# Performance work log

Hardware: AMD Instinct MI355X
Metric: run time of the kernel (lower is better)

Reference implementation:

```python
import jax, jax.numpy as jnp
import numpy as np

STRIDE = 4
N_LAYERS = 4
N_HEADS = 8
D_MODEL = 1024
D_FF = 4096
WINDOW = 400 // STRIDE      # lookback window (in folded frames)
LOOKFWD = 80 // STRIDE      # lookforward (in folded frames)
ROPE_BASE = 10000.0


def _layernorm(x, scale, bias, eps=1e-5):
    mu = jnp.mean(x, axis=-1, keepdims=True)
    var = jnp.mean(jnp.square(x - mu), axis=-1, keepdims=True)
    return (x - mu) * jax.lax.rsqrt(var + eps) * scale + bias


def _rope(x):
    # x: [B, H, S, Dh]
    B, H, S, Dh = x.shape
    half = Dh // 2
    inv_freq = 1.0 / (ROPE_BASE ** (jnp.arange(half, dtype=jnp.float32) / half))
    ang = jnp.arange(S, dtype=jnp.float32)[:, None] * inv_freq[None, :]  # [S, half]
    cos = jnp.cos(ang).astype(x.dtype)
    sin = jnp.sin(ang).astype(x.dtype)
    x1, x2 = x[..., :half], x[..., half:]
    return jnp.concatenate([x1 * cos - x2 * sin, x1 * sin + x2 * cos], axis=-1)


def setup_inputs() -> dict:
    key = jax.random.key(0)
    ks = jax.random.split(key, 32)
    B, T, C = 4, 4096, 512
    L, D, F = N_LAYERS, D_MODEL, D_FF
    s = 0.02
    inp = {
        'x': jax.random.normal(ks[0], (B, T, C), dtype=jnp.float32),
        'x_lengths': jax.random.randint(ks[1], (B,), 0, T + 1, dtype=jnp.int64 if jax.config.jax_enable_x64 else jnp.int32),
        'Wp': jax.random.normal(ks[2], (C * STRIDE, D), dtype=jnp.float32) * s,
        'bp': jnp.zeros((D,), jnp.float32),
        'ln1_s': jnp.ones((L, D), jnp.float32), 'ln1_b': jnp.zeros((L, D), jnp.float32),
        'Wq': jax.random.normal(ks[3], (L, D, D), jnp.float32) * s, 'bq': jnp.zeros((L, D), jnp.float32),
        'Wk': jax.random.normal(ks[4], (L, D, D), jnp.float32) * s, 'bk': jnp.zeros((L, D), jnp.float32),
        'Wv': jax.random.normal(ks[5], (L, D, D), jnp.float32) * s, 'bv': jnp.zeros((L, D), jnp.float32),
        'Wo': jax.random.normal(ks[6], (L, D, D), jnp.float32) * s, 'bo': jnp.zeros((L, D), jnp.float32),
        'ln2_s': jnp.ones((L, D), jnp.float32), 'ln2_b': jnp.zeros((L, D), jnp.float32),
        'W1': jax.random.normal(ks[7], (L, D, F), jnp.float32) * s, 'b1': jnp.zeros((L, F), jnp.float32),
        'W2': jax.random.normal(ks[8], (L, F, D), jnp.float32) * s, 'b2': jnp.zeros((L, D), jnp.float32),
        'lnf_s': jnp.ones((D,), jnp.float32), 'lnf_b': jnp.zeros((D,), jnp.float32),
    }
    return inp


def reference(x, x_lengths, Wp, bp, ln1_s, ln1_b, Wq, bq, Wk, bk, Wv, bv, Wo, bo,
              ln2_s, ln2_b, W1, b1, W2, b2, lnf_s, lnf_b):
    B, T, C = x.shape
    S = T // STRIDE
    H, Dh = N_HEADS, D_MODEL // N_HEADS
    # stride-fold + input projection
    xf = x[:, :S * STRIDE].reshape(B, S, C * STRIDE)
    h = xf @ Wp + bp                                  # [B, S, D]
    lens = x_lengths // STRIDE
    pad = (jnp.arange(S)[None, :] < lens[:, None])    # [B, S] valid-key mask
    h = h * pad[:, :, None].astype(h.dtype)
    # sliding-window causal-with-lookforward mask + key padding
    i = jnp.arange(S)[:, None]
    j = jnp.arange(S)[None, :]
    win = (j - i <= LOOKFWD) & (i - j < WINDOW)       # [S, S]
    allowed = win[None, None] & pad[:, None, None, :] # [B, 1, S, S]
    bias = jnp.where(allowed, 0.0, -1e9).astype(h.dtype)
    scale = 1.0 / jnp.sqrt(jnp.asarray(Dh, h.dtype))
    for l in range(N_LAYERS):
        # --- pre-LN RoPE windowed attention ---
        y = _layernorm(h, ln1_s[l], ln1_b[l])
        q = (y @ Wq[l] + bq[l]).reshape(B, S, H, Dh).transpose(0, 2, 1, 3)
        k = (y @ Wk[l] + bk[l]).reshape(B, S, H, Dh).transpose(0, 2, 1, 3)
        v = (y @ Wv[l] + bv[l]).reshape(B, S, H, Dh).transpose(0, 2, 1, 3)
        q, k = _rope(q), _rope(k)
        scores = jnp.einsum('bhqe,bhke->bhqk', q, k) * scale + bias
        attn = jax.nn.softmax(scores, axis=-1)
        ctx = jnp.einsum('bhqk,bhke->bhqe', attn, v)
        ctx = ctx.transpose(0, 2, 1, 3).reshape(B, S, D_MODEL)
        h = h + ctx @ Wo[l] + bo[l]
        # --- pre-LN FFN (kernel_size=1 conv == linear), swish ---
        y = _layernorm(h, ln2_s[l], ln2_b[l])
        h = h + jax.nn.silu(y @ W1[l] + b1[l]) @ W2[l] + b2[l]
    return _layernorm(h, lnf_s, lnf_b)
```

## Files before the change

### kernel.cpp

```cpp
#include <hip/hip_runtime.h>
#include <hip/hip_bf16.h>
#include <math.h>

typedef __hip_bfloat16 bf16;
typedef __attribute__((ext_vector_type(8))) short short8;
typedef __attribute__((ext_vector_type(4))) float f32x4;

#define S_LEN 1024
#define BATCH 4
#define M_ROWS 4096
#define DMODEL 1024
#define DFF 4096
#define NHEAD 8
#define DHEAD 128
#define WIN 100
#define LFWD 20

__device__ __forceinline__ void gl_lds16(const void* g, void* l) {
    __builtin_amdgcn_global_load_lds(
        (const __attribute__((address_space(1))) void*)g,
        (__attribute__((address_space(3))) void*)l, 16, 0, 0);
}

__device__ __forceinline__ float bf2f(unsigned short u) {
    return __uint_as_float(((unsigned)u) << 16);
}

__device__ __forceinline__ int xcd_swz(int flat, int nb) {
    return (flat & 7) * (nb >> 3) + (flat >> 3);
}

template<typename TC>
__global__ __launch_bounds__(256)
void mfma_gemm(const bf16* __restrict__ A, const bf16* __restrict__ Bt,
               const float* __restrict__ bias, TC* __restrict__ C,
               int M, int N, int K, int act)
{
    __shared__ bf16 As[2][128 * 32];
    __shared__ bf16 Bs[2][128 * 32];
    const int gx = gridDim.x;
    const int nb = gx * gridDim.y;
    const int swz = xcd_swz(blockIdx.x + gx * blockIdx.y, nb);
    const int bn = (swz % gx) * 128;
    const int bm = (swz / gx) * 128;
    const int tid = threadIdx.x;
    const int w = tid >> 6, lane = tid & 63;
    const int wm = (w & 1) * 64, wn = (w >> 1) * 64;

    const int srow = w * 32 + (lane >> 2);
    const int selem = (lane & 3) * 8;
    const bf16* ga0 = A + (size_t)(bm + srow) * K + selem;
    const bf16* ga1 = ga0 + (size_t)16 * K;
    const bf16* gb0 = Bt + (size_t)(bn + srow) * K + selem;
    const bf16* gb1 = gb0 + (size_t)16 * K;
    const int l0 = (w * 32) * 32;
    const int l1 = (w * 32 + 16) * 32;

    f32x4 acc[4][4] = {};
    const int koff = (lane >> 4) * 8;
    const int fr = lane & 15;

    gl_lds16(ga0, As[0] + l0); gl_lds16(ga1, As[0] + l1);
    gl_lds16(gb0, Bs[0] + l0); gl_lds16(gb1, Bs[0] + l1);
    ga0 += 32; ga1 += 32; gb0 += 32; gb1 += 32;
    __syncthreads();

    const int nk = K >> 5;
    int cur = 0;
    for (int t = 0; t < nk; ++t) {
        if (t + 1 < nk) {
            bf16* a = As[cur ^ 1]; bf16* b = Bs[cur ^ 1];
            gl_lds16(ga0, a + l0); gl_lds16(ga1, a + l1);
            gl_lds16(gb0, b + l0); gl_lds16(gb1, b + l1);
            ga0 += 32; ga1 += 32; gb0 += 32; gb1 += 32;
        }
        short8 af[4], bfr[4];
#pragma unroll
        for (int i = 0; i < 4; ++i)
            af[i] = *(const short8*)(As[cur] + (wm + i * 16 + fr) * 32 + koff);
#pragma unroll
        for (int j = 0; j < 4; ++j)
            bfr[j] = *(const short8*)(Bs[cur] + (wn + j * 16 + fr) * 32 + koff);
#pragma unroll
        for (int i = 0; i < 4; ++i)
#pragma unroll
            for (int j = 0; j < 4; ++j)
                acc[i][j] = __builtin_amdgcn_mfma_f32_16x16x32_bf16(
                    af[i], bfr[j], acc[i][j], 0, 0, 0);
        __syncthreads();
        cur ^= 1;
    }

    const int cq = lane >> 4, cn = lane & 15;
#pragma unroll
    for (int i = 0; i < 4; ++i) {
#pragma unroll
        for (int r = 0; r < 4; ++r) {
            int row = bm + wm + i * 16 + cq * 4 + r;
#pragma unroll
            for (int j = 0; j < 4; ++j) {
                int col = bn + wn + j * 16 + cn;
                float v = acc[i][j][r] + bias[col];
                if (act) v = v / (1.0f + __expf(-v));
                C[(size_t)row * N + col] = (TC)v;
            }
        }
    }
}

__global__ __launch_bounds__(256)
void mfma_gemm_sk(const bf16* __restrict__ A, const bf16* __restrict__ Bt,
                  const float* __restrict__ bias, float* __restrict__ C,
                  const float* __restrict__ resid,
                  float* __restrict__ P0, float* __restrict__ P1, int prows0,
                  int M, int N, int K)
{
    __shared__ bf16 As[2][128 * 32];
    __shared__ bf16 Bs[2][128 * 32];
    const int gx = gridDim.x, gy = gridDim.y;
    const int nb = gx * gy * 2;
    const int swz = xcd_swz(blockIdx.x + gx * (blockIdx.y + gy * blockIdx.z), nb);
    const int bn = (swz % gx) * 128;
    const int bm = ((swz / gx) % gy) * 128;
    const int z  = swz / (gx * gy);
    const int khalf = K >> 1;
    const int kstart = z * khalf;
    const int tid = threadIdx.x;
    const int w = tid >> 6, lane = tid & 63;
    const int wm = (w & 1) * 64, wn = (w >> 1) * 64;

    const int srow = w * 32 + (lane >> 2);
    const int selem = (lane & 3) * 8;
    const bf16* ga0 = A + (size_t)(bm + srow) * K + kstart + selem;
    const bf16* ga1 = ga0 + (size_t)16 * K;
    const bf16* gb0 = Bt + (size_t)(bn + srow) * K + kstart + selem;
    const bf16* gb1 = gb0 + (size_t)16 * K;
    const int l0 = (w * 32) * 32;
    const int l1 = (w * 32 + 16) * 32;

    f32x4 acc[4][4] = {};
    const int koff = (lane >> 4) * 8;
    const int fr = lane & 15;

    gl_lds16(ga0, As[0] + l0); gl_lds16(ga1, As[0] + l1);
    gl_lds16(gb0, Bs[0] + l0); gl_lds16(gb1, Bs[0] + l1);
    ga0 += 32; ga1 += 32; gb0 += 32; gb1 += 32;
    __syncthreads();

    const int nk = khalf >> 5;
    int cur = 0;
    for (int t = 0; t < nk; ++t) {
        if (t + 1 < nk) {
            bf16* a = As[cur ^ 1]; bf16* b = Bs[cur ^ 1];
            gl_lds16(ga0, a + l0); gl_lds16(ga1, a + l1);
            gl_lds16(gb0, b + l0); gl_lds16(gb1, b + l1);
            ga0 += 32; ga1 += 32; gb0 += 32; gb1 += 32;
        }
        short8 af[4], bfr[4];
#pragma unroll
        for (int i = 0; i < 4; ++i)
            af[i] = *(const short8*)(As[cur] + (wm + i * 16 + fr) * 32 + koff);
#pragma unroll
        for (int j = 0; j < 4; ++j)
            bfr[j] = *(const short8*)(Bs[cur] + (wn + j * 16 + fr) * 32 + koff);
#pragma unroll
        for (int i = 0; i < 4; ++i)
#pragma unroll
            for (int j = 0; j < 4; ++j)
                acc[i][j] = __builtin_amdgcn_mfma_f32_16x16x32_bf16(
                    af[i], bfr[j], acc[i][j], 0, 0, 0);
        __syncthreads();
        cur ^= 1;
    }

    const int cq = lane >> 4, cn = lane & 15;
#pragma unroll
    for (int i = 0; i < 4; ++i) {
#pragma unroll
        for (int r = 0; r < 4; ++r) {
            int row = bm + wm + i * 16 + cq * 4 + r;
#pragma unroll
            for (int j = 0; j < 4; ++j) {
                int col = bn + wn + j * 16 + cn;
                float v = acc[i][j][r];
                if (z == 0) {
                    v += bias[col];
                    if (resid) v += resid[(size_t)row * N + col];
                    C[(size_t)row * N + col] = v;
                } else {
                    float* P = (row < prows0) ? (P0 + (size_t)row * N + col)
                                              : (P1 + (size_t)(row - prows0) * N + col);
                    *P = v;
                }
            }
        }
    }
}

__global__ void transpose_kernel(const float* __restrict__ W, bf16* __restrict__ Wt,
                                 int K, int N, int ld)
{
    __shared__ float t[32][33];
    const int n0 = blockIdx.x * 32, k0 = blockIdx.y * 32;
    const int tx = threadIdx.x & 31, ty = threadIdx.x >> 5;
#pragma unroll
    for (int i = 0; i < 32; i += 8)
        t[ty + i][tx] = W[(size_t)(k0 + ty + i) * ld + n0 + tx];
    __syncthreads();
#pragma unroll
    for (int i = 0; i < 32; i += 8)
        Wt[(size_t)(n0 + ty + i) * K + k0 + tx] = (bf16)t[tx][ty + i];
}

__global__ void cvt_kernel(const float* __restrict__ s, bf16* __restrict__ d)
{
    size_t i = ((size_t)blockIdx.x * 256 + threadIdx.x) * 4;
    float4 v = *(const float4*)(s + i);
    d[i] = (bf16)v.x; d[i + 1] = (bf16)v.y; d[i + 2] = (bf16)v.z; d[i + 3] = (bf16)v.w;
}

__global__ void concat3_kernel(const float* __restrict__ a, const float* __restrict__ b,
                               const float* __restrict__ c, float* __restrict__ o)
{
    int i = blockIdx.x * 256 + threadIdx.x;
    o[i] = (i < 1024) ? a[i] : (i < 2048 ? b[i - 1024] : c[i - 2048]);
}

__global__ void pad_red_kernel(float* __restrict__ h, const float* __restrict__ P,
                               const int* __restrict__ xlen)
{
    int row = blockIdx.x;
    int b = row >> 10, s = row & 1023;
    int len = xlen[b] >> 2;
    size_t off = (size_t)row * DMODEL;
    if (s >= len) {
        for (int d = threadIdx.x; d < DMODEL; d += 256) h[off + d] = 0.0f;
    } else {
        for (int d = threadIdx.x; d < DMODEL; d += 256) h[off + d] += P[off + d];
    }
}

__global__ void reduce2_kernel(float* __restrict__ h, const float* __restrict__ P0,
                               const float* __restrict__ P1, int prows0)
{
    int row = blockIdx.x;
    const float* P = (row < prows0) ? (P0 + (size_t)row * DMODEL)
                                    : (P1 + (size_t)(row - prows0) * DMODEL);
    size_t off = (size_t)row * DMODEL;
#pragma unroll
    for (int t = 0; t < 4; ++t) {
        int d = threadIdx.x + 256 * t;
        h[off + d] += P[d];
    }
}

template<typename TO, bool RED>
__global__ void ln_kernel(float* __restrict__ x, const float* __restrict__ P0,
                          const float* __restrict__ sc, const float* __restrict__ bi,
                          TO* __restrict__ y)
{
    int row = blockIdx.x;
    float* xr = x + (size_t)row * DMODEL;
    const float* pr = RED ? (P0 + (size_t)row * DMODEL) : nullptr;
    float vals[4];
    float lsum = 0.0f, lsq = 0.0f;
#pragma unroll
    for (int t = 0; t < 4; ++t) {
        int d = threadIdx.x + 256 * t;
        float v = xr[d];
        if (RED) { v += pr[d]; xr[d] = v; }
        vals[t] = v; lsum += v; lsq += v * v;
    }
    for (int o = 32; o > 0; o >>= 1) {
        lsum += __shfl_down(lsum, o, 64);
        lsq  += __shfl_down(lsq,  o, 64);
    }
    __shared__ float s1[4], s2[4];
    int wv = threadIdx.x >> 6, ln = threadIdx.x & 63;
    if (ln == 0) { s1[wv] = lsum; s2[wv] = lsq; }
    __syncthreads();
    if (threadIdx.x == 0) {
        float a = s1[0] + s1[1] + s1[2] + s1[3];
        float b = s2[0] + s2[1] + s2[2] + s2[3];
        float mu = a * (1.0f / DMODEL);
        float var = b * (1.0f / DMODEL) - mu * mu;
        s1[0] = mu;
        s2[0] = rsqrtf(fmaxf(var, 0.0f) + 1e-5f);
    }
    __syncthreads();
    float mu = s1[0], inv = s2[0];
#pragma unroll
    for (int t = 0; t < 4; ++t) {
        int d = threadIdx.x + 256 * t;
        y[(size_t)row * DMODEL + d] = (TO)((vals[t] - mu) * inv * sc[d] + bi[d]);
    }
}

__global__ void rope_kernel(bf16* __restrict__ q, bf16* __restrict__ k, int stride)
{
    size_t idx = (size_t)blockIdx.x * 256 + threadIdx.x;
    int d = idx & 63;
    size_t rest = idx >> 6;
    int hh = rest & 7;
    int s = (rest >> 3) & 1023;
    size_t base = (rest >> 3) * stride + (size_t)hh * DHEAD;
    float inv = exp2f((float)d * -0.20762050593045235f);
    float ang = (float)s * inv;
    float c, si;
    __sincosf(ang, &si, &c);
    {
        float x1 = (float)q[base + d], x2 = (float)q[base + 64 + d];
        q[base + d]      = (bf16)(x1 * c - x2 * si);
        q[base + 64 + d] = (bf16)(x1 * si + x2 * c);
    }
    {
        float x1 = (float)k[base + d], x2 = (float)k[base + 64 + d];
        k[base + d]      = (bf16)(x1 * c - x2 * si);
        k[base + 64 + d] = (bf16)(x1 * si + x2 * c);
    }
}

__global__ void vmean_part(const bf16* __restrict__ v, float* __restrict__ part,
                           int stride)
{
    int g = blockIdx.x;
    int chunk = g & 31;
    int bh = g >> 5;
    int b = bh >> 3, hh = bh & 7;
    int d = threadIdx.x;
    const bf16* base = v + ((size_t)(b * S_LEN + chunk * 32)) * stride
                         + hh * DHEAD + d;
    float acc = 0.0f;
#pragma unroll 4
    for (int s = 0; s < 32; ++s)
        acc += (float)base[(size_t)s * stride];
    part[((size_t)bh * 32 + chunk) * DHEAD + d] = acc;
}

__global__ void vmean_fin(const float* __restrict__ part, float* __restrict__ vmean)
{
    int bh = blockIdx.x;
    int d = threadIdx.x;
    float acc = 0.0f;
#pragma unroll
    for (int c = 0; c < 32; ++c)
        acc += part[((size_t)bh * 32 + c) * DHEAD + d];
    vmean[(size_t)bh * DHEAD + d] = acc * (1.0f / S_LEN);
}

__global__ void attn_kernel(const bf16* __restrict__ q, const bf16* __restrict__ k,
                            const bf16* __restrict__ v, const float* __restrict__ vmean,
                            const int* __restrict__ xlen, bf16* __restrict__ ctx,
                            int stride)
{
    const int lane = threadIdx.x;
    int bhi = blockIdx.x;
    int i = bhi & 1023;
    int hh = (bhi >> 10) & 7;
    int b = bhi >> 13;
    int len = xlen[b] >> 2;
    size_t rowQ = ((size_t)(b * S_LEN + i)) * stride + hh * DHEAD;
    size_t rowC = ((size_t)(b * S_LEN + i)) * DMODEL + hh * DHEAD;
    int j0 = i - (WIN - 1); if (j0 < 0) j0 = 0;
    if (j0 >= len) {
        const float* vm = vmean + (size_t)(b * NHEAD + hh) * DHEAD;
        ctx[rowC + 2 * lane]     = (bf16)vm[2 * lane];
        ctx[rowC + 2 * lane + 1] = (bf16)vm[2 * lane + 1];
        return;
    }
    int j1 = i + LFWD; if (j1 > S_LEN - 1) j1 = S_LEN - 1;
    if (j1 > len - 1) j1 = len - 1;

    __shared__ float qs[DHEAD];
    __shared__ float p[128];
    qs[lane]      = (float)q[rowQ + lane];
    qs[lane + 64] = (float)q[rowQ + 64 + lane];
    __syncthreads();

    const float scale = 0.088388347648318447f;
    int jA = j0 + lane, jB = j0 + 64 + lane;
    float s0 = -1e30f, s1 = -1e30f;
    if (jA <= j1) {
        const short8* kr = (const short8*)(k + ((size_t)(b * S_LEN + jA)) * stride + hh * DHEAD);
        float acc = 0.0f;
#pragma unroll
        for (int c = 0; c < 16; ++c) {
            short8 kk = kr[c];
#pragma unroll
            for (int t = 0; t < 8; ++t)
                acc += qs[c * 8 + t] * bf2f((unsigned short)kk[t]);
        }
        s0 = acc * scale;
    }
    if (jB <= j1) {
        const short8* kr = (const short8*)(k + ((size_t)(b * S_LEN + jB)) * stride + hh * DHEAD);
        float acc = 0.0f;
#pragma unroll
        for (int c = 0; c < 16; ++c) {
            short8 kk = kr[c];
#pragma unroll
            for (int t = 0; t < 8; ++t)
                acc += qs[c * 8 + t] * bf2f((unsigned short)kk[t]);
        }
        s1 = acc * scale;
    }
    float m = fmaxf(s0, s1);
    for (int o = 32; o > 0; o >>= 1) m = fmaxf(m, __shfl_down(m, o, 64));
    m = __shfl(m, 0, 64);
    float e0 = (jA <= j1) ? __expf(s0 - m) : 0.0f;
    float e1 = (jB <= j1) ? __expf(s1 - m) : 0.0f;
    float ssum = e0 + e1;
    for (int o = 32; o > 0; o >>= 1) ssum += __shfl_down(ssum, o, 64);
    ssum = __shfl(ssum, 0, 64);
    float inv = 1.0f / fmaxf(ssum, 1e-30f);
    p[lane] = e0 * inv;
    p[lane + 64] = e1 * inv;
    __syncthreads();

    float a0 = 0.0f, a1 = 0.0f;
    for (int j = j0; j <= j1; ++j) {
        float pj = p[j - j0];
        const unsigned* vr = (const unsigned*)(v + ((size_t)(b * S_LEN + j)) * stride + hh * DHEAD);
        unsigned u = vr[lane];
        a0 += pj * bf2f((unsigned short)(u & 0xffff));
        a1 += pj * bf2f((unsigned short)(u >> 16));
    }
    ctx[rowC + 2 * lane]     = (bf16)a0;
    ctx[rowC + 2 * lane + 1] = (bf16)a1;
}

extern "C" void kernel_launch(void* const* d_in, const int* in_sizes, int n_in,
                              void* d_out, int out_size, void* d_ws, size_t ws_size,
                              hipStream_t stream)
{
    const float* x      = (const float*)d_in[0];
    const int*   xlen   = (const int*)d_in[1];
    const float* Wp     = (const float*)d_in[2];
    const float* bp     = (const float*)d_in[3];
    const float* ln1_s  = (const float*)d_in[4];
    const float* ln1_b  = (const float*)d_in[5];
    const float* Wq     = (const float*)d_in[6];
    const float* bq     = (const float*)d_in[7];
    const float* Wk     = (const float*)d_in[8];
    const float* bk     = (const float*)d_in[9];
    const float* Wv     = (const float*)d_in[10];
    const float* bv     = (const float*)d_in[11];
    const float* Wo     = (const float*)d_in[12];
    const float* bo     = (const float*)d_in[13];
    const float* ln2_s  = (const float*)d_in[14];
    const float* ln2_b  = (const float*)d_in[15];
    const float* W1     = (const float*)d_in[16];
    const float* b1     = (const float*)d_in[17];
    const float* W2     = (const float*)d_in[18];
    const float* b2     = (const float*)d_in[19];
    const float* lnf_s  = (const float*)d_in[20];
    const float* lnf_b  = (const float*)d_in[21];
    (void)in_sizes; (void)n_in; (void)out_size; (void)ws_size;

    const size_t MD = (size_t)M_ROWS * DMODEL;
    float* h     = (float*)d_ws;
    bf16*  y     = (bf16*)(h + MD);
    float* yfP   = (float*)(h + MD);
    bf16*  U     = y + MD;
    bf16*  xb    = U;
    bf16*  qkv   = U;
    bf16*  mid   = U;
    float* UfP   = (float*)U;
    float* UfP2  = (float*)(U + 8 * 1024 * 1024);
    float* vmean = (float*)(U + 16 * 1024 * 1024);
    float* bqkv  = vmean + BATCH * NHEAD * DHEAD;
    bf16*  wt    = (bf16*)d_out;
    float* doP   = (float*)((char*)d_out + 8 * 1024 * 1024);
    float* vpart = doP;

    const int QS = 3 * DMODEL;

    dim3 blk(256);
    dim3 gSK(DMODEL / 128, M_ROWS / 128, 2);

    cvt_kernel<<<(2 * MD) / (256 * 4), blk, 0, stream>>>(x, xb);
    transpose_kernel<<<dim3(DMODEL / 32, 2048 / 32), blk, 0, stream>>>(Wp, wt, 2048, DMODEL, DMODEL);
    mfma_gemm_sk<<<gSK, blk, 0, stream>>>(xb, wt, bp, h, nullptr,
                                          UfP2, nullptr, M_ROWS, M_ROWS, DMODEL, 2048);
    pad_red_kernel<<<M_ROWS, blk, 0, stream>>>(h, UfP2, xlen);

    for (int l = 0; l < 4; ++l) {
        const size_t wD  = (size_t)l * DMODEL * DMODEL;
        const size_t wF  = (size_t)l * DMODEL * DFF;
        const size_t wF2 = (size_t)l * DFF * DMODEL;
        const size_t vD  = (size_t)l * DMODEL;
        const size_t vF  = (size_t)l * DFF;

        ln_kernel<bf16, false><<<M_ROWS, blk, 0, stream>>>(h, nullptr,
                                                           ln1_s + vD, ln1_b + vD, y);

        transpose_kernel<<<dim3(32, 32), blk, 0, stream>>>(Wq + wD, wt, DMODEL, DMODEL, DMODEL);
        transpose_kernel<<<dim3(32, 32), blk, 0, stream>>>(Wk + wD, wt + MD / 4, DMODEL, DMODEL, DMODEL);
        transpose_kernel<<<dim3(32, 32), blk, 0, stream>>>(Wv + wD, wt + MD / 2, DMODEL, DMODEL, DMODEL);
        concat3_kernel<<<12, blk, 0, stream>>>(bq + vD, bk + vD, bv + vD, bqkv);
        mfma_gemm<bf16><<<dim3(3 * DMODEL / 128, M_ROWS / 128), blk, 0, stream>>>(
            y, wt, bqkv, qkv, M_ROWS, 3 * DMODEL, DMODEL, 0);

        bf16* qb = qkv;
        bf16* kb = qkv + DMODEL;
        bf16* vb = qkv + 2 * DMODEL;
        rope_kernel<<<(M_ROWS * NHEAD * 64) / 256, blk, 0, stream>>>(qb, kb, QS);
        vmean_part<<<BATCH * NHEAD * 32, dim3(DHEAD), 0, stream>>>(vb, vpart, QS);
        vmean_fin<<<BATCH * NHEAD, dim3(DHEAD), 0, stream>>>(vpart, vmean);
        attn_kernel<<<BATCH * NHEAD * S_LEN, dim3(64), 0, stream>>>(qb, kb, vb, vmean,
                                                                    xlen, y, QS);

        transpose_kernel<<<dim3(32, 32), blk, 0, stream>>>(Wo + wD, wt, DMODEL, DMODEL, DMODEL);
        mfma_gemm_sk<<<gSK, blk, 0, stream>>>(y, wt, bo + vD, h, h,
                                              UfP, nullptr, M_ROWS, M_ROWS, DMODEL, 1024);

        ln_kernel<bf16, true><<<M_ROWS, blk, 0, stream>>>(h, UfP,
                                                          ln2_s + vD, ln2_b + vD, y);

        transpose_kernel<<<dim3(DFF / 32, DMODEL / 32), blk, 0, stream>>>(
            W1 + wF, wt, DMODEL, DFF, DFF);
        mfma_gemm<bf16><<<dim3(DFF / 128, M_ROWS / 128), blk, 0, stream>>>(
            y, wt, b1 + vF, mid, M_ROWS, DFF, DMODEL, 1);

        transpose_kernel<<<dim3(DMODEL / 32, DFF / 32), blk, 0, stream>>>(
            W2 + wF2, wt, DFF, DMODEL, DMODEL);
        mfma_gemm_sk<<<gSK, blk, 0, stream>>>(mid, wt, b2 + vD, h, h,
                                              yfP, doP, 2048, M_ROWS, DMODEL, DFF);
        reduce2_kernel<<<M_ROWS, blk, 0, stream>>>(h, yfP, doP, 2048);
    }

    ln_kernel<float, false><<<M_ROWS, blk, 0, stream>>>(h, nullptr, lnf_s, lnf_b,
                                                        (float*)d_out);
}
```

Measured before the change: 1.698 ms.

## Rewrite windowed attention as tiled MFMA kernel with transposed V staging

Replaces the per-query scalar attention kernel with a block-tiled kernel that computes 32 queries per block using bf16 MFMA for both QK^T and PV, with double-buffered K/V tiles loaded via global-to-LDS copies and XOR swizzling. A new transpose kernel writes V as [bh, d, s] into a scratch region so PV fragments can be loaded contiguously. This removes redundant K/V reloads across neighbouring queries and scalar FMA work. In exchange it adds an extra transpose pass and rounds the probabilities to bf16.

```diff
diff --git a/kernel.cpp b/kernel.cpp
--- a/kernel.cpp
+++ b/kernel.cpp
@@ -210,6 +210,23 @@
 #pragma unroll
     for (int i = 0; i < 32; i += 8)
         Wt[(size_t)(n0 + ty + i) * K + k0 + tx] = (bf16)t[tx][ty + i];
+}
+
+__global__ void vtrans_kernel(const bf16* __restrict__ qkv, bf16* __restrict__ vt)
+{
+    __shared__ bf16 t[32][33];
+    const int bh = blockIdx.z;
+    const int s0 = blockIdx.x * 32, d0 = blockIdx.y * 32;
+    const int b = bh >> 3, h = bh & 7;
+    const int tx = threadIdx.x & 31, ty = threadIdx.x >> 5;
+#pragma unroll
+    for (int i = 0; i < 32; i += 8)
+        t[ty + i][tx] = qkv[(size_t)(b * S_LEN + s0 + ty + i) * 3072 + 2048
+                            + h * DHEAD + d0 + tx];
+    __syncthreads();
+#pragma unroll
+    for (int i = 0; i < 32; i += 8)
+        vt[(size_t)(bh * DHEAD + d0 + ty + i) * 1024 + s0 + tx] = t[tx][ty + i];
 }
 
 __global__ void cvt_kernel(const float* __restrict__ s, bf16* __restrict__ d)
@@ -348,85 +365,183 @@
     vmean[(size_t)bh * DHEAD + d] = acc * (1.0f / S_LEN);
 }
 
-__global__ void attn_kernel(const bf16* __restrict__ q, const bf16* __restrict__ k,
-                            const bf16* __restrict__ v, const float* __restrict__ vmean,
-                            const int* __restrict__ xlen, bf16* __restrict__ ctx,
-                            int stride)
-{
-    const int lane = threadIdx.x;
-    int bhi = blockIdx.x;
-    int i = bhi & 1023;
-    int hh = (bhi >> 10) & 7;
-    int b = bhi >> 13;
-    int len = xlen[b] >> 2;
-    size_t rowQ = ((size_t)(b * S_LEN + i)) * stride + hh * DHEAD;
-    size_t rowC = ((size_t)(b * S_LEN + i)) * DMODEL + hh * DHEAD;
-    int j0 = i - (WIN - 1); if (j0 < 0) j0 = 0;
-    if (j0 >= len) {
-        const float* vm = vmean + (size_t)(b * NHEAD + hh) * DHEAD;
-        ctx[rowC + 2 * lane]     = (bf16)vm[2 * lane];
-        ctx[rowC + 2 * lane + 1] = (bf16)vm[2 * lane + 1];
-        return;
-    }
-    int j1 = i + LFWD; if (j1 > S_LEN - 1) j1 = S_LEN - 1;
-    if (j1 > len - 1) j1 = len - 1;
-
-    __shared__ float qs[DHEAD];
-    __shared__ float p[128];
-    qs[lane]      = (float)q[rowQ + lane];
-    qs[lane + 64] = (float)q[rowQ + 64 + lane];
-    __syncthreads();
+__global__ __launch_bounds__(128)
+void attn_mfma(const bf16* __restrict__ qkv, const bf16* __restrict__ vt_g,
+               const float* __restrict__ vmean, const int* __restrict__ xlen,
+               bf16* __restrict__ ctx)
+{
+    __shared__ bf16 KV[2][64 * 128];
+    __shared__ bf16 P[2][16 * 192];
+
+    const int qt = blockIdx.x;
+    const int bh = blockIdx.y;
+    const int b = bh >> 3, h = bh & 7;
+    const int tid = threadIdx.x;
+    const int w = tid >> 6, l = tid & 63;
+    const int qlo = qt * 32;
+    const int len = xlen[b] >> 2;
+
+    int s0 = qlo - 128; if (s0 < 0) s0 = 0;
+    const int jmax = qlo + 51;
+    int k0t[3]; int nt = 0;
+#pragma unroll
+    for (int t = 0; t < 3; ++t) {
+        int k0 = s0 + t * 64;
+        if (k0 <= jmax && k0 < len) { k0t[nt] = k0; ++nt; }
+    }
+
+    const bf16* qbase = qkv + (size_t)(b * S_LEN) * 3072 + h * DHEAD;
+    const bf16* kbase = qbase + DMODEL;
+
+    short8 qa[4];
+    {
+        const bf16* qr = qbase + (size_t)(qlo + w * 16 + (l & 15)) * 3072 + (l >> 4) * 8;
+#pragma unroll
+        for (int kk = 0; kk < 4; ++kk)
+            qa[kk] = *(const short8*)(qr + kk * 32);
+    }
+
+    auto stageK = [&](int k0, int buf) {
+#pragma unroll
+        for (int c = 0; c < 8; ++c) {
+            int rl = w * 32 + c * 4 + (l >> 4);
+            int sr = k0 + rl; if (sr > S_LEN - 1) sr = S_LEN - 1;
+            int sc = ((l & 15) * 8) ^ ((rl & 7) << 3);
+            gl_lds16(kbase + (size_t)sr * 3072 + sc,
+                     &KV[buf][(w * 32 + c * 4) * 128]);
+        }
+    };
+    auto stageV = [&](int k0, int buf) {
+#pragma unroll
+        for (int c = 0; c < 8; ++c) {
+            int d = w * 64 + c * 8 + (l >> 3);
+            int js = ((l & 7) * 8) ^ ((d & 7) << 3);
+            int s = k0 + js; if (s > S_LEN - 8) s = S_LEN - 8;
+            gl_lds16(vt_g + (size_t)(bh * 128 + d) * 1024 + s,
+                     &KV[buf][(w * 64 + c * 8) * 64]);
+        }
+    };
+
+    f32x4 sf[3][4] = {};
+
+    auto sphase = [&](int t, int buf) {
+#pragma unroll
+        for (int jb = 0; jb < 4; ++jb) {
+            int row = jb * 16 + (l & 15);
+#pragma unroll
+            for (int kk = 0; kk < 4; ++kk) {
+                int kel = (kk * 32 + (l >> 4) * 8) ^ ((row & 7) << 3);
+                short8 kf = *(const short8*)(&KV[buf][row * 128 + kel]);
+                sf[t][jb] = __builtin_amdgcn_mfma_f32_16x16x32_bf16(
+                    qa[kk], kf, sf[t][jb], 0, 0, 0);
+            }
+        }
+    };
+
+    if (nt > 0) stageK(k0t[0], 0);
+    __syncthreads();
+    if (nt > 1) stageK(k0t[1], 1);
+    if (nt > 0) sphase(0, 0);
+    __syncthreads();
+    if (nt > 2) stageK(k0t[2], 0);
+    if (nt > 1) sphase(1, 1);
+    __syncthreads();
+    if (nt > 2) sphase(2, 0);
+    if (nt > 0) stageV(k0t[0], 1);
 
     const float scale = 0.088388347648318447f;
-    int jA = j0 + lane, jB = j0 + 64 + lane;
-    float s0 = -1e30f, s1 = -1e30f;
-    if (jA <= j1) {
-        const short8* kr = (const short8*)(k + ((size_t)(b * S_LEN + jA)) * stride + hh * DHEAD);
-        float acc = 0.0f;
-#pragma unroll
-        for (int c = 0; c < 16; ++c) {
-            short8 kk = kr[c];
-#pragma unroll
-            for (int t = 0; t < 8; ++t)
-                acc += qs[c * 8 + t] * bf2f((unsigned short)kk[t]);
-        }
-        s0 = acc * scale;
-    }
-    if (jB <= j1) {
-        const short8* kr = (const short8*)(k + ((size_t)(b * S_LEN + jB)) * stride + hh * DHEAD);
-        float acc = 0.0f;
-#pragma unroll
-        for (int c = 0; c < 16; ++c) {
-            short8 kk = kr[c];
-#pragma unroll
-            for (int t = 0; t < 8; ++t)
-                acc += qs[c * 8 + t] * bf2f((unsigned short)kk[t]);
-        }
-        s1 = acc * scale;
-    }
-    float m = fmaxf(s0, s1);
-    for (int o = 32; o > 0; o >>= 1) m = fmaxf(m, __shfl_down(m, o, 64));
-    m = __shfl(m, 0, 64);
-    float e0 = (jA <= j1) ? __expf(s0 - m) : 0.0f;
-    float e1 = (jB <= j1) ? __expf(s1 - m) : 0.0f;
-    float ssum = e0 + e1;
-    for (int o = 32; o > 0; o >>= 1) ssum += __shfl_down(ssum, o, 64);
-    ssum = __shfl(ssum, 0, 64);
-    float inv = 1.0f / fmaxf(ssum, 1e-30f);
-    p[lane] = e0 * inv;
-    p[lane + 64] = e1 * inv;
-    __syncthreads();
-
-    float a0 = 0.0f, a1 = 0.0f;
-    for (int j = j0; j <= j1; ++j) {
-        float pj = p[j - j0];
-        const unsigned* vr = (const unsigned*)(v + ((size_t)(b * S_LEN + j)) * stride + hh * DHEAD);
-        unsigned u = vr[lane];
-        a0 += pj * bf2f((unsigned short)(u & 0xffff));
-        a1 += pj * bf2f((unsigned short)(u >> 16));
-    }
-    ctx[rowC + 2 * lane]     = (bf16)a0;
-    ctx[rowC + 2 * lane + 1] = (bf16)a1;
+    float mr[4] = {-1e30f, -1e30f, -1e30f, -1e30f};
+#pragma unroll
+    for (int t = 0; t < 3; ++t) if (t < nt) {
+#pragma unroll
+        for (int jb = 0; jb < 4; ++jb) {
+            int j = k0t[t] + jb * 16 + (l & 15);
+            bool jok = (j < len);
+#pragma unroll
+            for (int r = 0; r < 4; ++r) {
+                int i = qlo + w * 16 + ((l >> 4) << 2) + r;
+                float v = sf[t][jb][r] * scale;
+                bool ok = jok && (j - i <= LFWD) && (i - j < WIN);
+                v = ok ? v : -1e30f;
+                sf[t][jb][r] = v;
+                mr[r] = fmaxf(mr[r], v);
+            }
+        }
+    }
+#pragma unroll
+    for (int o = 1; o <= 8; o <<= 1)
+#pragma unroll
+        for (int r = 0; r < 4; ++r)
+            mr[r] = fmaxf(mr[r], __shfl_xor(mr[r], o, 64));
+
+    float lr[4] = {0.0f, 0.0f, 0.0f, 0.0f};
+#pragma unroll
+    for (int t = 0; t < 3; ++t) if (t < nt) {
+#pragma unroll
+        for (int jb = 0; jb < 4; ++jb) {
+#pragma unroll
+            for (int r = 0; r < 4; ++r) {
+                int q = ((l >> 4) << 2) + r;
+                int jrel = t * 64 + jb * 16 + (l & 15);
+                float e = __expf(sf[t][jb][r] - mr[r]);
+                lr[r] += e;
+                P[w][q * 192 + (jrel ^ ((q & 7) << 3))] = (bf16)e;
+            }
+        }
+    }
+#pragma unroll
+    for (int o = 1; o <= 8; o <<= 1)
+#pragma unroll
+        for (int r = 0; r < 4; ++r)
+            lr[r] += __shfl_xor(lr[r], o, 64);
+    float inv[4];
+#pragma unroll
+    for (int r = 0; r < 4; ++r) inv[r] = 1.0f / fmaxf(lr[r], 1e-30f);
+
+    __syncthreads();
+
+    f32x4 acc[8] = {};
+    auto pv = [&](int ti, int buf) {
+#pragma unroll
+        for (int s32 = 0; s32 < 2; ++s32) {
+            int q = l & 15;
+            int jr8 = ti * 64 + s32 * 32 + (l >> 4) * 8;
+            short8 pa = *(const short8*)(&P[w][q * 192 + (jr8 ^ ((q & 7) << 3))]);
+#pragma unroll
+            for (int db = 0; db < 8; ++db) {
+                int d = db * 16 + (l & 15);
+                int je = (s32 * 32 + (l >> 4) * 8) ^ ((d & 7) << 3);
+                short8 vf = *(const short8*)(&KV[buf][d * 64 + je]);
+                acc[db] = __builtin_amdgcn_mfma_f32_16x16x32_bf16(
+                    pa, vf, acc[db], 0, 0, 0);
+            }
+        }
+    };
+
+    if (nt > 1) stageV(k0t[1], 0);
+    if (nt > 0) pv(0, 1);
+    __syncthreads();
+    if (nt > 2) stageV(k0t[2], 1);
+    if (nt > 1) pv(1, 0);
+    __syncthreads();
+    if (nt > 2) pv(2, 1);
+
+    const float* vm = vmean + (size_t)bh * DHEAD;
+    float vmr[8];
+#pragma unroll
+    for (int db = 0; db < 8; ++db) vmr[db] = vm[db * 16 + (l & 15)];
+#pragma unroll
+    for (int r = 0; r < 4; ++r) {
+        int i = qlo + w * 16 + ((l >> 4) << 2) + r;
+        bf16* crow = ctx + (size_t)(b * S_LEN + i) * DMODEL + h * DHEAD;
+        bool em = mr[r] < -1e29f;
+        float iv = inv[r];
+#pragma unroll
+        for (int db = 0; db < 8; ++db) {
+            float v = em ? vmr[db] : acc[db][r] * iv;
+            crow[db * 16 + (l & 15)] = (bf16)v;
+        }
+    }
 }
 
 extern "C" void kernel_launch(void* const* d_in, const int* in_sizes, int n_in,
@@ -472,7 +587,7 @@
     bf16*  wt    = (bf16*)d_out;
     float* doP   = (float*)((char*)d_out + 8 * 1024 * 1024);
     float* vpart = doP;
-
+    bf16*  vt_g  = (bf16*)d_out;
     const int QS = 3 * DMODEL;
 
     dim3 blk(256);
@@ -505,10 +620,10 @@
         bf16* kb = qkv + DMODEL;
         bf16* vb = qkv + 2 * DMODEL;
         rope_kernel<<<(M_ROWS * NHEAD * 64) / 256, blk, 0, stream>>>(qb, kb, QS);
+        vtrans_kernel<<<dim3(32, 4, 32), blk, 0, stream>>>(qkv, vt_g);
         vmean_part<<<BATCH * NHEAD * 32, dim3(DHEAD), 0, stream>>>(vb, vpart, QS);
         vmean_fin<<<BATCH * NHEAD, dim3(DHEAD), 0, stream>>>(vpart, vmean);
-        attn_kernel<<<BATCH * NHEAD * S_LEN, dim3(64), 0, stream>>>(qb, kb, vb, vmean,
-                                                                    xlen, y, QS);
+        attn_mfma<<<dim3(32, 32), dim3(128), 0, stream>>>(qkv, vt_g, vmean, xlen, y);
 
         transpose_kernel<<<dim3(32, 32), blk, 0, stream>>>(Wo + wD, wt, DMODEL, DMODEL, DMODEL);
         mfma_gemm_sk<<<gSK, blk, 0, stream>>>(y, wt, bo + vD, h, h,
```

After: 1.466 ms. -13.7%, faster.
